# Performance work log

Hardware: AMD Instinct MI355X
Metric: run time of the kernel (lower is better)

## Reference

```python
import jax, jax.numpy as jnp
import numpy as np

B, R, S = 4, 16384, 96
NEAR, FAR = 2.0, 6.0

def setup_inputs() -> dict:
    key = jax.random.key(0)
    k1, k2, k3 = jax.random.split(key, 3)
    colors = jax.random.normal(k1, (B, R, S, 3), dtype=jnp.float32)
    densities = jax.random.normal(k2, (B, R, S, 1), dtype=jnp.float32)
    # depths must be monotonically increasing along the sample axis
    depths = jnp.sort(
        NEAR + (FAR - NEAR) * jax.random.uniform(k3, (B, R, S, 1), dtype=jnp.float32),
        axis=2,
    )
    return {"colors": colors, "densities": densities, "depths": depths, "white_back": 0}


def reference(colors, densities, depths, white_back):
    dtype = colors.dtype
    # midpoint (Mip-NeRF style) quantities along the sample axis (dim 2)
    deltas = depths[:, :, 1:] - depths[:, :, :-1]            # [B,R,S-1,1]
    colors_mid = (colors[:, :, :-1] + colors[:, :, 1:]) * 0.5  # [B,R,S-1,3]
    densities_mid = (densities[:, :, :-1] + densities[:, :, 1:]) * 0.5
    depths_mid = (depths[:, :, :-1] + depths[:, :, 1:]) * 0.5

    densities_mid = jax.nn.softplus(densities_mid).astype(dtype)  # activation_factory
    density_delta = densities_mid * deltas
    alpha = (1.0 - jnp.exp(-density_delta)).astype(dtype)         # [B,R,S-1,1]

    # transmittance via cumulative product of shifted (1 - alpha)
    alpha_shifted = jnp.concatenate(
        [jnp.ones_like(alpha[:, :, :1]), 1.0 - alpha + 1e-10], axis=2
    )
    weights = (alpha * jnp.cumprod(alpha_shifted, axis=2)[:, :, :-1]).astype(dtype)

    composite_rgb = jnp.sum(weights * colors_mid, axis=2)   # [B,R,3]
    weight_total = jnp.sum(weights, axis=2)                 # [B,R,1]
    composite_depth = jnp.sum(weights * depths_mid, axis=2) # [B,R,1]
    composite_depth = jnp.nan_to_num(composite_depth, nan=jnp.inf).astype(dtype)
    composite_depth = jnp.clip(composite_depth, jnp.min(depths), jnp.max(depths))

    if white_back:
        composite_rgb = composite_rgb + 1.0 - weight_total
    return composite_rgb, composite_depth, weights
```

## Files before the change

### kernel.cpp

```cpp
#include <hip/hip_runtime.h>
#include <math.h>

#define S 96
#define SM 95
#define WPB 16
#define L2E 1.4426950408889634f

__device__ __forceinline__ float fexp2(float x) {
#if __has_builtin(__builtin_amdgcn_exp2f)
    return __builtin_amdgcn_exp2f(x);
#else
    return exp2f(x);
#endif
}
__device__ __forceinline__ float flog2(float x) {
#if __has_builtin(__builtin_amdgcn_logf)
    return __builtin_amdgcn_logf(x);
#else
    return log2f(x);
#endif
}

template <int CTRL, int RMASK>
__device__ __forceinline__ float updpp0(float src) {
    return __int_as_float(__builtin_amdgcn_update_dpp(
        0, __float_as_int(src), CTRL, RMASK, 0xF, false));
}

__device__ __forceinline__ float dpp_scan_add(float x) {
    x += updpp0<0x111, 0xF>(x);
    x += updpp0<0x112, 0xF>(x);
    x += updpp0<0x114, 0xF>(x);
    x += updpp0<0x118, 0xF>(x);
    x += updpp0<0x142, 0xA>(x);
    x += updpp0<0x143, 0xC>(x);
    return x;
}

__device__ __forceinline__ float rdlane(float x, int lane) {
    return __int_as_float(__builtin_amdgcn_readlane(__float_as_int(x), lane));
}
__device__ __forceinline__ float wave_sum(float x) {
    return rdlane(dpp_scan_add(x), 63);
}
__device__ __forceinline__ float wshr1(float x) { return updpp0<0x138, 0xF>(x); }
__device__ __forceinline__ float wshl1(float x) { return updpp0<0x130, 0xF>(x); }

__global__ void init_ws_kernel(unsigned int* ws) {
    ws[0] = 0x7F800000u;
    ws[1] = 0xFF800000u;
}

template <bool SLOT>
__global__ __launch_bounds__(WPB * 64) void march_kernel(
    const float* __restrict__ colors,
    const float* __restrict__ dens,
    const float* __restrict__ depths,
    const int* __restrict__ white_back,
    unsigned int* __restrict__ ws,
    float* __restrict__ out_rgb,
    float* __restrict__ out_dep,
    float* __restrict__ out_w,
    int nrays, int nblocks) {
    __shared__ float smn[WPB], smx[WPB];
    const int wv = threadIdx.x >> 6;
    const int l = threadIdx.x & 63;
    const int ray0 = blockIdx.x * WPB + wv;
    const bool valid = (ray0 < nrays);
    const int ray = valid ? ray0 : (nrays - 1);
    const int wb = *white_back;

    const float* db = depths + (size_t)ray * S;
    const float* sb = dens + (size_t)ray * S;
    const float3* cb3 = (const float3*)(colors + (size_t)ray * (3 * S));

    float d_a = db[l];
    float s_a = sb[l];
    float3 ca = cb3[l];
    const bool hb = (l < 32);
    float d_b = 0.f, s_b = 0.f;
    float3 cbv = {0.f, 0.f, 0.f};
    if (hb) {
        d_b = db[64 + l];
        s_b = sb[64 + l];
        cbv = cb3[64 + l];
    }

    float rmn = rdlane(d_a, 0);
    float rmx = rdlane(d_b, 31);
    if (!valid) { rmn = INFINITY; rmx = -INFINITY; }
    if (l == 0) { smn[wv] = rmn; smx[wv] = rmx; }
    __syncthreads();
    if (threadIdx.x == 0) {
        float bmn = smn[0], bmx = smx[0];
#pragma unroll
        for (int i = 1; i < WPB; ++i) {
            bmn = fminf(bmn, smn[i]);
            bmx = fmaxf(bmx, smx[i]);
        }
        if (SLOT) {
            float* sl = (float*)ws;
            sl[blockIdx.x] = bmn;
            sl[nblocks + blockIdx.x] = bmx;
        } else {
            atomicMin((int*)&ws[0], __float_as_int(bmn));
            atomicMax((int*)&ws[1], __float_as_int(bmx));
        }
    }

    float dn_a = wshl1(d_a);
    float sn_a = wshl1(s_a);
    {
        float d64 = rdlane(d_b, 0);
        float s64 = rdlane(s_b, 0);
        if (l == 63) { dn_a = d64; sn_a = s64; }
    }
    float dn_b = wshl1(d_b);
    float sn_b = wshl1(s_b);

    const float C1 = 0.5f * L2E;
    float x_a = (s_a + sn_a) * C1;
    float lg_a = fmaxf(x_a, 0.f) + flog2(1.f + fexp2(-fabsf(x_a)));
    float dd_a = (dn_a - d_a) * lg_a;
    float x_b = (s_b + sn_b) * C1;
    float lg_b = fmaxf(x_b, 0.f) + flog2(1.f + fexp2(-fabsf(x_b)));
    float dd_b = (l <= 30) ? (dn_b - d_b) * lg_b : 0.f;

    float A = dpp_scan_add(dd_a);
    float P = rdlane(A, 63);
    float Bc = dpp_scan_add(dd_b);

    float Ti_a = fexp2(-A);
    float Ti_b = fexp2(-(P + Bc));
    float T63 = rdlane(Ti_a, 62);
    float T64 = rdlane(Ti_a, 63);
    float T95 = rdlane(Ti_b, 31);

    float Te_a = wshr1(Ti_a);
    if (l == 0) Te_a = 1.f;
    float Te_b = wshr1(Ti_b);
    if (l == 0) Te_b = T64;
    float Tm1_a = wshr1(Te_a);
    if (l == 0) Tm1_a = 1.f;
    float Tm1_b = wshr1(Te_b);
    if (l == 0) Tm1_b = T63;

    float w_a = Te_a - Ti_a;
    float w_b = Te_b - Ti_b;
    float v_a = 0.5f * (Tm1_a - Ti_a);
    float v_b = hb ? 0.5f * (Tm1_b - Ti_b) : 0.f;

    float r_sum = wave_sum(v_a * ca.x + v_b * cbv.x);
    float g_sum = wave_sum(v_a * ca.y + v_b * cbv.y);
    float b_sum = wave_sum(v_a * ca.z + v_b * cbv.z);
    float dep_sum = wave_sum(v_a * d_a + v_b * d_b);

    if (!valid) return;

    float* wout = out_w + (size_t)ray * SM;
    wout[l] = w_a;
    if (l <= 30) wout[64 + l] = w_b;

    if (l == 0) {
        float rr = r_sum, gg = g_sum, bb = b_sum;
        if (wb) { rr += T95; gg += T95; bb += T95; }
        out_rgb[(size_t)ray * 3 + 0] = rr;
        out_rgb[(size_t)ray * 3 + 1] = gg;
        out_rgb[(size_t)ray * 3 + 2] = bb;
        float cd = dep_sum;
        if (isnan(cd)) cd = INFINITY;
        out_dep[ray] = cd;
    }
}

__global__ __launch_bounds__(256) void tail_kernel(
    float* __restrict__ dep, const unsigned int* __restrict__ ws,
    int n, int nblocks, int slotMode) {
    float gmn, gmx;
    if (slotMode) {
        const float* sl = (const float*)ws;
        float mn = INFINITY, mx = -INFINITY;
        const int nv = nblocks >> 2;
        const float4* mn4 = (const float4*)sl;
        const float4* mx4 = (const float4*)(sl + nblocks);
        for (int i = threadIdx.x; i < nv; i += 256) {
            float4 a = mn4[i];
            float4 b = mx4[i];
            mn = fminf(mn, fminf(fminf(a.x, a.y), fminf(a.z, a.w)));
            mx = fmaxf(mx, fmaxf(fmaxf(b.x, b.y), fmaxf(b.z, b.w)));
        }
        for (int i = (nv << 2) + threadIdx.x; i < nblocks; i += 256) {
            mn = fminf(mn, sl[i]);
            mx = fmaxf(mx, sl[nblocks + i]);
        }
#pragma unroll
        for (int off = 32; off >= 1; off >>= 1) {
            mn = fminf(mn, __shfl_xor(mn, off));
            mx = fmaxf(mx, __shfl_xor(mx, off));
        }
        __shared__ float a[4], b[4];
        const int wv = threadIdx.x >> 6;
        if ((threadIdx.x & 63) == 0) { a[wv] = mn; b[wv] = mx; }
        __syncthreads();
        gmn = fminf(fminf(a[0], a[1]), fminf(a[2], a[3]));
        gmx = fmaxf(fmaxf(b[0], b[1]), fmaxf(b[2], b[3]));
    } else {
        gmn = __int_as_float((int)ws[0]);
        gmx = __int_as_float((int)ws[1]);
    }
    int i = blockIdx.x * 256 + threadIdx.x;
    if (i < n) dep[i] = fminf(fmaxf(dep[i], gmn), gmx);
}

extern "C" void kernel_launch(void* const* d_in, const int* in_sizes, int n_in,
                              void* d_out, int out_size, void* d_ws, size_t ws_size,
                              hipStream_t stream) {
    const float* colors = (const float*)d_in[0];
    const float* dens = (const float*)d_in[1];
    const float* depths = (const float*)d_in[2];
    const int* white_back = (const int*)d_in[3];

    const int nrays = in_sizes[1] / S;
    unsigned int* ws = (unsigned int*)d_ws;

    float* out_rgb = (float*)d_out;
    float* out_dep = out_rgb + (size_t)nrays * 3;
    float* out_w = out_dep + nrays;

    const int nblocks = (nrays + WPB - 1) / WPB;
    const bool slot = ws_size >= (size_t)(2 * nblocks) * sizeof(float);

    if (slot) {
        march_kernel<true><<<nblocks, WPB * 64, 0, stream>>>(
            colors, dens, depths, white_back, ws, out_rgb, out_dep, out_w,
            nrays, nblocks);
    } else {
        init_ws_kernel<<<1, 1, 0, stream>>>(ws);
        march_kernel<false><<<nblocks, WPB * 64, 0, stream>>>(
            colors, dens, depths, white_back, ws, out_rgb, out_dep, out_w,
            nrays, nblocks);
    }
    tail_kernel<<<(nrays + 255) / 256, 256, 0, stream>>>(
        out_dep, ws, nrays, nblocks, slot ? 1 : 0);
}
```

Baseline: 33.33 us.

## Map two rays per wavefront with three samples per lane

Each 64-lane wave now handles two rays, one per 32-lane half, and each lane owns three consecutive samples loaded as float3 vectors. The transmittance scan becomes a local serial sum followed by a 32-lane DPP scan, and the colour and depth reductions use the same half-wave scan read from lane 31. This is meant to remove the idle half-wave in the second sample chunk, halve the block count, and cut cross-lane operations. In exchange each lane makes strided float3 loads and stores, which may coalesce less well, and the 32-bit offset arithmetic assumes the sizes stay small.

```diff
diff --git a/kernel.cpp b/kernel.cpp
--- a/kernel.cpp
+++ b/kernel.cpp
@@ -27,21 +27,17 @@
         0, __float_as_int(src), CTRL, RMASK, 0xF, false));
 }
 
-__device__ __forceinline__ float dpp_scan_add(float x) {
+__device__ __forceinline__ float scan32(float x) {
     x += updpp0<0x111, 0xF>(x);
     x += updpp0<0x112, 0xF>(x);
     x += updpp0<0x114, 0xF>(x);
     x += updpp0<0x118, 0xF>(x);
     x += updpp0<0x142, 0xA>(x);
-    x += updpp0<0x143, 0xC>(x);
     return x;
 }
 
 __device__ __forceinline__ float rdlane(float x, int lane) {
     return __int_as_float(__builtin_amdgcn_readlane(__float_as_int(x), lane));
-}
-__device__ __forceinline__ float wave_sum(float x) {
-    return rdlane(dpp_scan_add(x), 63);
 }
 __device__ __forceinline__ float wshr1(float x) { return updpp0<0x138, 0xF>(x); }
 __device__ __forceinline__ float wshl1(float x) { return updpp0<0x130, 0xF>(x); }
@@ -65,30 +61,23 @@
     __shared__ float smn[WPB], smx[WPB];
     const int wv = threadIdx.x >> 6;
     const int l = threadIdx.x & 63;
-    const int ray0 = blockIdx.x * WPB + wv;
+    const int lp = l & 31;
+    const int ray0 = (blockIdx.x * WPB + wv) * 2 + (l >> 5);
     const bool valid = (ray0 < nrays);
     const int ray = valid ? ray0 : (nrays - 1);
     const int wb = *white_back;
 
-    const float* db = depths + (size_t)ray * S;
-    const float* sb = dens + (size_t)ray * S;
-    const float3* cb3 = (const float3*)(colors + (size_t)ray * (3 * S));
-
-    float d_a = db[l];
-    float s_a = sb[l];
-    float3 ca = cb3[l];
-    const bool hb = (l < 32);
-    float d_b = 0.f, s_b = 0.f;
-    float3 cbv = {0.f, 0.f, 0.f};
-    if (hb) {
-        d_b = db[64 + l];
-        s_b = sb[64 + l];
-        cbv = cb3[64 + l];
-    }
-
-    float rmn = rdlane(d_a, 0);
-    float rmx = rdlane(d_b, 31);
-    if (!valid) { rmn = INFINITY; rmx = -INFINITY; }
+    const int doff = ray * S + 3 * lp;
+    const int coff = ray * (3 * S) + 9 * lp;
+
+    const float3 dv = *(const float3*)(depths + doff);
+    const float3 sv = *(const float3*)(dens + doff);
+    const float3 ca = *(const float3*)(colors + coff);
+    const float3 cb = *(const float3*)(colors + coff + 3);
+    const float3 cc = *(const float3*)(colors + coff + 6);
+
+    float rmn = fminf(rdlane(dv.x, 0), rdlane(dv.x, 32));
+    float rmx = fmaxf(rdlane(dv.z, 31), rdlane(dv.z, 63));
     if (l == 0) { smn[wv] = rmn; smx[wv] = rmx; }
     __syncthreads();
     if (threadIdx.x == 0) {
@@ -108,66 +97,64 @@
         }
     }
 
-    float dn_a = wshl1(d_a);
-    float sn_a = wshl1(s_a);
-    {
-        float d64 = rdlane(d_b, 0);
-        float s64 = rdlane(s_b, 0);
-        if (l == 63) { dn_a = d64; sn_a = s64; }
-    }
-    float dn_b = wshl1(d_b);
-    float sn_b = wshl1(s_b);
+    float dn = wshl1(dv.x);
+    float sn = wshl1(sv.x);
 
     const float C1 = 0.5f * L2E;
-    float x_a = (s_a + sn_a) * C1;
-    float lg_a = fmaxf(x_a, 0.f) + flog2(1.f + fexp2(-fabsf(x_a)));
-    float dd_a = (dn_a - d_a) * lg_a;
-    float x_b = (s_b + sn_b) * C1;
-    float lg_b = fmaxf(x_b, 0.f) + flog2(1.f + fexp2(-fabsf(x_b)));
-    float dd_b = (l <= 30) ? (dn_b - d_b) * lg_b : 0.f;
-
-    float A = dpp_scan_add(dd_a);
-    float P = rdlane(A, 63);
-    float Bc = dpp_scan_add(dd_b);
-
-    float Ti_a = fexp2(-A);
-    float Ti_b = fexp2(-(P + Bc));
-    float T63 = rdlane(Ti_a, 62);
-    float T64 = rdlane(Ti_a, 63);
-    float T95 = rdlane(Ti_b, 31);
-
-    float Te_a = wshr1(Ti_a);
-    if (l == 0) Te_a = 1.f;
-    float Te_b = wshr1(Ti_b);
-    if (l == 0) Te_b = T64;
-    float Tm1_a = wshr1(Te_a);
-    if (l == 0) Tm1_a = 1.f;
-    float Tm1_b = wshr1(Te_b);
-    if (l == 0) Tm1_b = T63;
-
-    float w_a = Te_a - Ti_a;
-    float w_b = Te_b - Ti_b;
-    float v_a = 0.5f * (Tm1_a - Ti_a);
-    float v_b = hb ? 0.5f * (Tm1_b - Ti_b) : 0.f;
-
-    float r_sum = wave_sum(v_a * ca.x + v_b * cbv.x);
-    float g_sum = wave_sum(v_a * ca.y + v_b * cbv.y);
-    float b_sum = wave_sum(v_a * ca.z + v_b * cbv.z);
-    float dep_sum = wave_sum(v_a * d_a + v_b * d_b);
+    float x0 = (sv.x + sv.y) * C1;
+    float x1 = (sv.y + sv.z) * C1;
+    float x2 = (sv.z + sn) * C1;
+    float sp0 = fmaxf(x0, 0.f) + flog2(1.f + fexp2(-fabsf(x0)));
+    float sp1 = fmaxf(x1, 0.f) + flog2(1.f + fexp2(-fabsf(x1)));
+    float sp2 = fmaxf(x2, 0.f) + flog2(1.f + fexp2(-fabsf(x2)));
+    float dd0 = (dv.y - dv.x) * sp0;
+    float dd1 = (dv.z - dv.y) * sp1;
+    float dd2 = (lp < 31) ? (dn - dv.z) * sp2 : 0.f;
+
+    float cum1 = dd0 + dd1;
+    float cum2 = cum1 + dd2;
+    float incl = scan32(cum2);
+    float base = incl - cum2;
+
+    float T0 = fexp2(-base);
+    float T1 = fexp2(-(base + dd0));
+    float T2 = fexp2(-(base + cum1));
+    float T3 = fexp2(-incl);
+
+    float w0 = T0 - T1;
+    float w1 = T1 - T2;
+    float w2 = T2 - T3;
+
+    float Tm1 = wshr1(T2);
+    if (lp == 0) Tm1 = 1.f;
+    float v0 = Tm1 - T1;
+    float v1 = T0 - T2;
+    float v2 = T1 - T3;
+
+    float racc = v0 * ca.x + v1 * cb.x + v2 * cc.x;
+    float gacc = v0 * ca.y + v1 * cb.y + v2 * cc.y;
+    float bacc = v0 * ca.z + v1 * cb.z + v2 * cc.z;
+    float dacc = v0 * dv.x + v1 * dv.y + v2 * dv.z;
+    racc = scan32(racc);
+    gacc = scan32(gacc);
+    bacc = scan32(bacc);
+    dacc = scan32(dacc);
 
     if (!valid) return;
 
-    float* wout = out_w + (size_t)ray * SM;
-    wout[l] = w_a;
-    if (l <= 30) wout[64 + l] = w_b;
-
-    if (l == 0) {
-        float rr = r_sum, gg = g_sum, bb = b_sum;
+    const int woff = ray * SM + 3 * lp;
+    out_w[woff] = w0;
+    out_w[woff + 1] = w1;
+    if (lp < 31) out_w[woff + 2] = w2;
+
+    if (lp == 31) {
+        float T95 = T2;
+        float rr = 0.5f * racc, gg = 0.5f * gacc, bb = 0.5f * bacc;
         if (wb) { rr += T95; gg += T95; bb += T95; }
-        out_rgb[(size_t)ray * 3 + 0] = rr;
-        out_rgb[(size_t)ray * 3 + 1] = gg;
-        out_rgb[(size_t)ray * 3 + 2] = bb;
-        float cd = dep_sum;
+        out_rgb[ray * 3 + 0] = rr;
+        out_rgb[ray * 3 + 1] = gg;
+        out_rgb[ray * 3 + 2] = bb;
+        float cd = 0.5f * dacc;
         if (isnan(cd)) cd = INFINITY;
         out_dep[ray] = cd;
     }
@@ -227,7 +214,8 @@
     float* out_dep = out_rgb + (size_t)nrays * 3;
     float* out_w = out_dep + nrays;
 
-    const int nblocks = (nrays + WPB - 1) / WPB;
+    const int raysPB = 2 * WPB;
+    const int nblocks = (nrays + raysPB - 1) / raysPB;
     const bool slot = ws_size >= (size_t)(2 * nblocks) * sizeof(float);
 
     if (slot) {
```

After: 32.28 us. 3.1% less time.
